# Kernel optimization log

Measured on AMD Instinct MI355X. Metric: run time of the kernel, lower is better.

## Reference

```python
import jax, jax.numpy as jnp
import numpy as np

NUM_NODE = 100000
EMBED_DIM = 128
N_EDGES = 600000


def setup_inputs() -> dict:
    key = jax.random.key(0)
    k1, k2, k3, k4 = jax.random.split(key, 4)
    x = jax.random.normal(k1, (NUM_NODE, EMBED_DIM), dtype=jnp.float32)
    edge_index = jax.random.randint(k2, (2, N_EDGES), 0, NUM_NODE, dtype=jnp.int64)
    # nn.Linear(embed_dim, embed_dim): weight [out, in], bias [out]
    scale = 1.0 / np.sqrt(EMBED_DIM)
    W = jax.random.uniform(k3, (EMBED_DIM, EMBED_DIM), dtype=jnp.float32, minval=-scale, maxval=scale)
    b = jax.random.uniform(k4, (EMBED_DIM,), dtype=jnp.float32, minval=-scale, maxval=scale)
    return {"x": x, "edge_index": edge_index, "W": W, "b": b}


def reference(x, edge_index, W, b):
    source_nodes = edge_index[0]
    target_nodes = edge_index[1]
    # x_target = relu(Linear(x))  -- torch Linear: x @ W.T + b
    x_target = jax.nn.relu(x @ W.T + b)                      # [N, D]
    # scatter-add of gathered target features into source rows
    gathered = x_target[target_nodes]                        # [E, D]
    aggr = jax.ops.segment_sum(gathered, source_nodes, num_segments=NUM_NODE)  # [N, D]
    # degree normalization: bincount clamped to >= 1
    deg = jax.ops.segment_sum(jnp.ones((edge_index.shape[1],), dtype=jnp.float32),
                              source_nodes, num_segments=NUM_NODE)
    deg = jnp.maximum(deg, 1.0)
    return aggr / deg[:, None]
```

## Files before the change

### kernel.cpp

```cpp
#include <hip/hip_runtime.h>
#include <hip/hip_bf16.h>

typedef float f4 __attribute__((ext_vector_type(4)));
typedef float f32x4 __attribute__((ext_vector_type(4)));
typedef short bf16x8 __attribute__((ext_vector_type(8)));

#define D 128
#define SLOTS 96

__device__ __forceinline__ unsigned f2bf_u(float f) {
    unsigned u = __builtin_bit_cast(unsigned, f);
    unsigned r = 0x7FFFu + ((u >> 16) & 1u);
    return (u + r) >> 16;
}
__device__ __forceinline__ unsigned short f2bf(float f) {
    return (unsigned short)f2bf_u(f);
}
__device__ __forceinline__ float bf2f(short s) {
    unsigned u = ((unsigned)(unsigned short)s) << 16;
    return __builtin_bit_cast(float, u);
}

__global__ __launch_bounds__(256, 2) void gemm_mfma(
    const float* __restrict__ x, const float* __restrict__ W,
    const float* __restrict__ b, unsigned short* __restrict__ ybf,
    int* __restrict__ deg, int N)
{
    {
        int i = blockIdx.x * 256 + threadIdx.x;
        if (i < N) deg[i] = 0;
    }

    const int lane = threadIdx.x & 63;
    const int r16  = lane & 15;
    const int g4   = lane >> 4;
    const int gwave  = blockIdx.x * 4 + (threadIdx.x >> 6);
    const int nwaves = gridDim.x * 4;

    bf16x8 wfrag[8][4];
#pragma unroll
    for (int ct = 0; ct < 8; ++ct)
#pragma unroll
        for (int kf = 0; kf < 4; ++kf) {
            const float* wrow = W + (size_t)(16 * ct + r16) * D + kf * 32 + g4 * 8;
            f4 w0 = *reinterpret_cast<const f4*>(wrow);
            f4 w1 = *reinterpret_cast<const f4*>(wrow + 4);
            union { bf16x8 v; unsigned short s[8]; } wf;
#pragma unroll
            for (int e = 0; e < 8; ++e)
                wf.s[e] = f2bf(e < 4 ? w0[e] : w1[e - 4]);
            wfrag[ct][kf] = wf.v;
        }

    f4 bias4[8];
#pragma unroll
    for (int ct = 0; ct < 8; ++ct)
        bias4[ct] = *reinterpret_cast<const f4*>(b + 16 * ct + g4 * 4);

    const int ntiles = (N + 15) >> 4;
    int tile = gwave;
    if (tile >= ntiles) return;

    f4 xa[4][2];
    {
        int arow = tile * 16 + r16; if (arow >= N) arow = N - 1;
        const float* xr = x + (size_t)arow * D + g4 * 8;
#pragma unroll
        for (int kf = 0; kf < 4; ++kf) {
            xa[kf][0] = *reinterpret_cast<const f4*>(xr + kf * 32);
            xa[kf][1] = *reinterpret_cast<const f4*>(xr + kf * 32 + 4);
        }
    }

    while (true) {
        union { bf16x8 v; unsigned short s[8]; } afrag[4];
#pragma unroll
        for (int kf = 0; kf < 4; ++kf)
#pragma unroll
            for (int e = 0; e < 8; ++e)
                afrag[kf].s[e] = f2bf(e < 4 ? xa[kf][0][e] : xa[kf][1][e - 4]);

        const int next = tile + nwaves;
        const bool has_next = next < ntiles;
        if (has_next) {
            int arow = next * 16 + r16; if (arow >= N) arow = N - 1;
            const float* xr = x + (size_t)arow * D + g4 * 8;
#pragma unroll
            for (int kf = 0; kf < 4; ++kf) {
                xa[kf][0] = *reinterpret_cast<const f4*>(xr + kf * 32);
                xa[kf][1] = *reinterpret_cast<const f4*>(xr + kf * 32 + 4);
            }
        }

        const int row = tile * 16 + r16;
        unsigned short* yrow = ybf + (size_t)row * D + g4 * 4;
#pragma unroll
        for (int ct = 0; ct < 8; ++ct) {
            f32x4 acc = {0.f, 0.f, 0.f, 0.f};
#pragma unroll
            for (int kf = 0; kf < 4; ++kf)
                acc = __builtin_amdgcn_mfma_f32_16x16x32_bf16(
                    wfrag[ct][kf], afrag[kf].v, acc, 0, 0, 0);
            if (row < N) {
                float v0 = fmaxf(acc[0] + bias4[ct][0], 0.f);
                float v1 = fmaxf(acc[1] + bias4[ct][1], 0.f);
                float v2 = fmaxf(acc[2] + bias4[ct][2], 0.f);
                float v3 = fmaxf(acc[3] + bias4[ct][3], 0.f);
                uint2 o;
                o.x = f2bf_u(v0) | (f2bf_u(v1) << 16);
                o.y = f2bf_u(v2) | (f2bf_u(v3) << 16);
                *reinterpret_cast<uint2*>(yrow + 16 * ct) = o;
            }
        }

        if (!has_next) break;
        tile = next;
    }
}

__global__ __launch_bounds__(256) void scatter_hist_kernel(
    const int* __restrict__ src, const int* __restrict__ tgt,
    int* __restrict__ deg, int* __restrict__ slot, int E)
{
    int e = blockIdx.x * 256 + threadIdx.x;
    if (e < E) {
        int s = src[e];
        int p = atomicAdd(&deg[s], 1);
        slot[(size_t)s * SLOTS + p] = tgt[e];
    }
}

__global__ __launch_bounds__(256) void aggregate_bf16(
    const int* __restrict__ deg, const int* __restrict__ slot,
    const unsigned short* __restrict__ ybf, float* __restrict__ out, int N)
{
    const int g  = threadIdx.x >> 4;
    const int c8 = (threadIdx.x & 15) * 8;

    const int n = blockIdx.x * 16 + g;
    if (n >= N) return;
    const int d = deg[n];
    const int* sl = slot + (size_t)n * SLOTS;

    float a0[8] = {0,0,0,0,0,0,0,0}, a1[8] = {0,0,0,0,0,0,0,0};
    float a2[8] = {0,0,0,0,0,0,0,0}, a3[8] = {0,0,0,0,0,0,0,0};

    for (int j = 0; j < d; j += 4) {
        int4 tq = *reinterpret_cast<const int4*>(sl + j);
        if (j + 0 < d) {
            bf16x8 v = *reinterpret_cast<const bf16x8*>(ybf + (size_t)tq.x * D + c8);
#pragma unroll
            for (int e = 0; e < 8; ++e) a0[e] += bf2f(v[e]);
        }
        if (j + 1 < d) {
            bf16x8 v = *reinterpret_cast<const bf16x8*>(ybf + (size_t)tq.y * D + c8);
#pragma unroll
            for (int e = 0; e < 8; ++e) a1[e] += bf2f(v[e]);
        }
        if (j + 2 < d) {
            bf16x8 v = *reinterpret_cast<const bf16x8*>(ybf + (size_t)tq.z * D + c8);
#pragma unroll
            for (int e = 0; e < 8; ++e) a2[e] += bf2f(v[e]);
        }
        if (j + 3 < d) {
            bf16x8 v = *reinterpret_cast<const bf16x8*>(ybf + (size_t)tq.w * D + c8);
#pragma unroll
            for (int e = 0; e < 8; ++e) a3[e] += bf2f(v[e]);
        }
    }

    const float dinv = 1.0f / fmaxf((float)d, 1.f);
    f4 o0, o1;
#pragma unroll
    for (int e = 0; e < 4; ++e)
        o0[e] = ((a0[e] + a1[e]) + (a2[e] + a3[e])) * dinv;
#pragma unroll
    for (int e = 4; e < 8; ++e)
        o1[e - 4] = ((a0[e] + a1[e]) + (a2[e] + a3[e])) * dinv;

    float* orow = out + (size_t)n * D + c8;
    *reinterpret_cast<f4*>(orow)     = o0;
    *reinterpret_cast<f4*>(orow + 4) = o1;
}

extern "C" void kernel_launch(void* const* d_in, const int* in_sizes, int n_in,
                              void* d_out, int out_size, void* d_ws, size_t ws_size,
                              hipStream_t stream) {
    const float* x  = (const float*)d_in[0];
    const int*   ei = (const int*)d_in[1];
    const float* W  = (const float*)d_in[2];
    const float* b  = (const float*)d_in[3];
    float* out = (float*)d_out;

    const int N = in_sizes[0] / D;
    const int E = in_sizes[1] / 2;
    const int* src = ei;
    const int* tgt = ei + E;

    char* ws = (char*)d_ws;
    unsigned short* ybf = (unsigned short*)ws;   ws += (size_t)N * D * sizeof(unsigned short);
    int* deg  = (int*)ws;                        ws += (size_t)N * sizeof(int);
    int* slot = (int*)ws;                        ws += (size_t)N * SLOTS * sizeof(int);

    gemm_mfma<<<512, 256, 0, stream>>>(x, W, b, ybf, deg, N);

    int eb = (E + 255) / 256;
    scatter_hist_kernel<<<eb, 256, 0, stream>>>(src, tgt, deg, slot, E);

    int ab = (N + 15) / 16;
    aggregate_bf16<<<ab, 256, 0, stream>>>(deg, slot, ybf, out, N);
}
```

Baseline: 101.0 us.

## Stage bf16 weights in swizzled LDS shared per block instead of per-wave registers

Each block now converts W to bf16 once and stores it in LDS with an XOR swizzle. Each wave then reads its MFMA fragments from LDS per column tile, instead of every wave loading and converting all of W into registers. The bias also moves to LDS. Launch bounds rise to 3 blocks per SM, and the grid is sized from the tile count (about two tiles per wave) rather than fixed at 512 blocks. The aim is less redundant global W traffic and lower register pressure for higher occupancy, at the cost of extra LDS reads in the inner loop and an unrolled-1 column loop.

```diff
diff --git a/kernel.cpp b/kernel.cpp
--- a/kernel.cpp
+++ b/kernel.cpp
@@ -21,15 +21,40 @@
     return __builtin_bit_cast(float, u);
 }
 
-__global__ __launch_bounds__(256, 2) void gemm_mfma(
+__global__ __launch_bounds__(256, 3) void gemm_mfma(
     const float* __restrict__ x, const float* __restrict__ W,
     const float* __restrict__ b, unsigned short* __restrict__ ybf,
     int* __restrict__ deg, int N)
 {
+    __shared__ unsigned short Wl[D * D];
+    __shared__ float bl[D];
+
     {
         int i = blockIdx.x * 256 + threadIdx.x;
         if (i < N) deg[i] = 0;
     }
+
+    {
+        const int t = threadIdx.x;
+        const int r = t >> 1, h = t & 1;
+        const float* wr = W + (size_t)r * D + h * 64;
+        const unsigned swz = (unsigned)((r & 7) << 4);
+        char* lbase = (char*)Wl + r * 256;
+#pragma unroll
+        for (int j = 0; j < 8; ++j) {
+            f4 a = *reinterpret_cast<const f4*>(wr + j * 8);
+            f4 c = *reinterpret_cast<const f4*>(wr + j * 8 + 4);
+            uint4 o;
+            o.x = f2bf_u(a[0]) | (f2bf_u(a[1]) << 16);
+            o.y = f2bf_u(a[2]) | (f2bf_u(a[3]) << 16);
+            o.z = f2bf_u(c[0]) | (f2bf_u(c[1]) << 16);
+            o.w = f2bf_u(c[2]) | (f2bf_u(c[3]) << 16);
+            unsigned cb = (unsigned)(h * 128 + j * 16);
+            *reinterpret_cast<uint4*>(lbase + (cb ^ swz)) = o;
+        }
+        if (t < D) bl[t] = b[t];
+    }
+    __syncthreads();
 
     const int lane = threadIdx.x & 63;
     const int r16  = lane & 15;
@@ -37,25 +62,9 @@
     const int gwave  = blockIdx.x * 4 + (threadIdx.x >> 6);
     const int nwaves = gridDim.x * 4;
 
-    bf16x8 wfrag[8][4];
-#pragma unroll
-    for (int ct = 0; ct < 8; ++ct)
-#pragma unroll
-        for (int kf = 0; kf < 4; ++kf) {
-            const float* wrow = W + (size_t)(16 * ct + r16) * D + kf * 32 + g4 * 8;
-            f4 w0 = *reinterpret_cast<const f4*>(wrow);
-            f4 w1 = *reinterpret_cast<const f4*>(wrow + 4);
-            union { bf16x8 v; unsigned short s[8]; } wf;
-#pragma unroll
-            for (int e = 0; e < 8; ++e)
-                wf.s[e] = f2bf(e < 4 ? w0[e] : w1[e - 4]);
-            wfrag[ct][kf] = wf.v;
-        }
-
-    f4 bias4[8];
-#pragma unroll
-    for (int ct = 0; ct < 8; ++ct)
-        bias4[ct] = *reinterpret_cast<const f4*>(b + 16 * ct + g4 * 4);
+    const unsigned rbase = (unsigned)(r16 * 256);
+    const unsigned rswz  = (unsigned)((r16 & 7) << 4);
+    const unsigned gcb   = (unsigned)(g4 * 16);
 
     const int ntiles = (N + 15) >> 4;
     int tile = gwave;
@@ -94,18 +103,26 @@
 
         const int row = tile * 16 + r16;
         unsigned short* yrow = ybf + (size_t)row * D + g4 * 4;
-#pragma unroll
+#pragma unroll 1
         for (int ct = 0; ct < 8; ++ct) {
+            bf16x8 wf[4];
+#pragma unroll
+            for (int kf = 0; kf < 4; ++kf) {
+                unsigned off = (unsigned)(ct * 4096) + rbase
+                             + (((unsigned)(kf * 64) + gcb) ^ rswz);
+                wf[kf] = *reinterpret_cast<const bf16x8*>((const char*)Wl + off);
+            }
             f32x4 acc = {0.f, 0.f, 0.f, 0.f};
 #pragma unroll
             for (int kf = 0; kf < 4; ++kf)
                 acc = __builtin_amdgcn_mfma_f32_16x16x32_bf16(
-                    wfrag[ct][kf], afrag[kf].v, acc, 0, 0, 0);
+                    wf[kf], afrag[kf].v, acc, 0, 0, 0);
             if (row < N) {
-                float v0 = fmaxf(acc[0] + bias4[ct][0], 0.f);
-                float v1 = fmaxf(acc[1] + bias4[ct][1], 0.f);
-                float v2 = fmaxf(acc[2] + bias4[ct][2], 0.f);
-                float v3 = fmaxf(acc[3] + bias4[ct][3], 0.f);
+                f4 bias = *reinterpret_cast<const f4*>(bl + ct * 16 + g4 * 4);
+                float v0 = fmaxf(acc[0] + bias[0], 0.f);
+                float v1 = fmaxf(acc[1] + bias[1], 0.f);
+                float v2 = fmaxf(acc[2] + bias[2], 0.f);
+                float v3 = fmaxf(acc[3] + bias[3], 0.f);
                 uint2 o;
                 o.x = f2bf_u(v0) | (f2bf_u(v1) << 16);
                 o.y = f2bf_u(v2) | (f2bf_u(v3) << 16);
@@ -202,7 +219,9 @@
     int* deg  = (int*)ws;                        ws += (size_t)N * sizeof(int);
     int* slot = (int*)ws;                        ws += (size_t)N * SLOTS * sizeof(int);
 
-    gemm_mfma<<<512, 256, 0, stream>>>(x, W, b, ybf, deg, N);
+    int ntiles = (N + 15) / 16;
+    int gb = (ntiles + 7) / 8;
+    gemm_mfma<<<gb, 256, 0, stream>>>(x, W, b, ybf, deg, N);
 
     int eb = (E + 255) / 256;
     scatter_hist_kernel<<<eb, 256, 0, stream>>>(src, tgt, deg, slot, E);
```

After: 94.35 us. -6.6%, faster.
